# Kernel tuning notes

Hardware: AMD Instinct MI355X
Metric: run time of the kernel (lower is better)

Reference implementation:

```python
import jax, jax.numpy as jnp
import numpy as np

N = 100000      # num_nodes
E = 1600000     # num_edges (avg degree 16)
D_IN = 128
D_H = 128
D_OUT = 128


def _init_linear(key, out_dim, in_dim):
    # Kaiming-uniform-like init, bound = 1/sqrt(fan_in)
    bound = 1.0 / np.sqrt(in_dim)
    return jax.random.uniform(key, (out_dim, in_dim), jnp.float32, -bound, bound)


def setup_inputs() -> dict:
    key = jax.random.key(0)
    ks = jax.random.split(key, 12)
    x = jax.random.normal(ks[0], (N, D_IN), jnp.float32)
    edge_index = jax.random.randint(ks[1], (2, E), 0, N, jnp.int32)
    dims = [(D_H, D_IN), (D_H, D_H), (D_OUT, D_H)]
    inp = {"x": x, "edge_index": edge_index}
    for i, (do, di) in enumerate(dims):
        inp[f"Wl{i}"] = _init_linear(ks[2 + 3 * i], do, di)      # lin_l: applied to aggregated neighbors
        inp[f"bl{i}"] = jnp.zeros((do,), jnp.float32)
        inp[f"Wr{i}"] = _init_linear(ks[3 + 3 * i], do, di)      # lin_r: applied to root (self) features
    return inp


def _sage_conv(x, src, dst, Wl, bl, Wr):
    # mean aggregation of source-node features at destination nodes
    msg = x[src]                                                   # [E, d]
    agg = jax.ops.segment_sum(msg, dst, num_segments=N)            # [N, d]
    deg = jax.ops.segment_sum(jnp.ones((src.shape[0],), x.dtype), dst, num_segments=N)
    mean = agg / jnp.maximum(deg, 1.0)[:, None]
    return mean @ Wl.T + bl + x @ Wr.T


def reference(x, edge_index, Wl0, bl0, Wr0, Wl1, bl1, Wr1, Wl2, bl2, Wr2):
    src, dst = edge_index[0], edge_index[1]
    # dropout is identity in eval mode
    h = jax.nn.relu(_sage_conv(x, src, dst, Wl0, bl0, Wr0))
    h = jax.nn.relu(_sage_conv(h, src, dst, Wl1, bl1, Wr1))
    return _sage_conv(h, src, dst, Wl2, bl2, Wr2)
```

## Files before the change

### kernel.cpp

```cpp
#include <hip/hip_runtime.h>
#include <hip/hip_bf16.h>

typedef __attribute__((ext_vector_type(8))) short bf16x8;
typedef __attribute__((ext_vector_type(4))) float f32x4;

#define D 128
#define P2CAP 8192


__global__ __launch_bounds__(256) void k_setup(
    const float* __restrict__ x,
    const float* __restrict__ w0, const float* __restrict__ w1,
    const float* __restrict__ w2, const float* __restrict__ w3,
    const float* __restrict__ w4, const float* __restrict__ w5,
    __hip_bfloat16* __restrict__ xb, __hip_bfloat16* __restrict__ wb,
    int* __restrict__ bhist, int xpair)
{
    int t = blockIdx.x * 256 + threadIdx.x;
    if (t < 512) bhist[t] = 0;
    if (t < xpair) {
        float2 f = ((const float2*)x)[t];
        ((__hip_bfloat162*)xb)[t] = __float22bfloat162_rn(f);
    }
    if (t < 6 * 8192) {
        int wsel = t >> 13, wi = t & 8191;
        const float* wp = w0;
        if (wsel == 1) wp = w1;
        else if (wsel == 2) wp = w2;
        else if (wsel == 3) wp = w3;
        else if (wsel == 4) wp = w4;
        else if (wsel == 5) wp = w5;
        float2 f = ((const float2*)wp)[wi];
        ((__hip_bfloat162*)wb)[t] = __float22bfloat162_rn(f);
    }
}


__global__ __launch_bounds__(256) void k_p0(const int* __restrict__ dst,
                                            int* __restrict__ bhist, int e, int n, int epb) {
    __shared__ int lh[512];
    for (int i = threadIdx.x; i < 512; i += 256) lh[i] = 0;
    __syncthreads();
    int lo = blockIdx.x * epb;
    int hi = lo + epb; if (hi > e) hi = e;
    for (int i = lo + threadIdx.x; i < hi; i += 256) {
        int d = dst[i]; d = ((unsigned)d < (unsigned)n) ? d : 0;
        atomicAdd(&lh[d >> 8], 1);
    }
    __syncthreads();
    for (int i = threadIdx.x; i < 512; i += 256)
        if (lh[i]) atomicAdd(&bhist[i], lh[i]);
}

__global__ void k_bscan(const int* __restrict__ bhist, int* __restrict__ bbase,
                        int* __restrict__ bcursor, int nb) {
    __shared__ int lds[512];
    int t = threadIdx.x;
    int v = (t < nb) ? bhist[t] : 0;
    lds[t] = v;
    __syncthreads();
    for (int off = 1; off < 512; off <<= 1) {
        int x = (t >= off) ? lds[t - off] : 0;
        __syncthreads();
        lds[t] += x;
        __syncthreads();
    }
    if (t < nb) { int b = lds[t] - v; bbase[t] = b; bcursor[t] = b; }
    if (t == nb) bbase[t] = lds[nb - 1];
}

__global__ __launch_bounds__(256) void k_p1(const int* __restrict__ src,
                                            const int* __restrict__ dst,
                                            int* __restrict__ bcursor,
                                            int* __restrict__ tmp, int e, int n, int epb) {
    __shared__ int lh[512], gb[512];
    for (int i = threadIdx.x; i < 512; i += 256) lh[i] = 0;
    __syncthreads();
    int lo = blockIdx.x * epb;
    int hi = lo + epb; if (hi > e) hi = e;
    for (int i = lo + threadIdx.x; i < hi; i += 256) {
        int d = dst[i]; d = ((unsigned)d < (unsigned)n) ? d : 0;
        atomicAdd(&lh[d >> 8], 1);
    }
    __syncthreads();
    for (int i = threadIdx.x; i < 512; i += 256) {
        int c = lh[i];
        gb[i] = c ? atomicAdd(&bcursor[i], c) : 0;
    }
    __syncthreads();
    for (int i = threadIdx.x; i < 512; i += 256) lh[i] = 0;
    __syncthreads();
    for (int i = lo + threadIdx.x; i < hi; i += 256) {
        int d = dst[i]; d = ((unsigned)d < (unsigned)n) ? d : 0;
        int s = src[i]; s = ((unsigned)s < (unsigned)n) ? s : 0;
        int b = d >> 8;
        int p = gb[b] + atomicAdd(&lh[b], 1);
        tmp[p] = s | ((d & 255) << 17);
    }
}

__global__ __launch_bounds__(256) void k_p2(const int* __restrict__ tmp,
                                            const int* __restrict__ bbase,
                                            int* __restrict__ deg, int* __restrict__ offs,
                                            int* __restrict__ csr, int n) {
    __shared__ int hist[256], loc[256], cur[256];
    __shared__ int out[P2CAP];
    int b = blockIdx.x, t = threadIdx.x;
    int base = bbase[b];
    int cnt = bbase[b + 1] - base;
    int nodes = n - b * 256; if (nodes > 256) nodes = 256;
    hist[t] = 0;
    __syncthreads();
    for (int i = t; i < cnt; i += 256)
        atomicAdd(&hist[(tmp[base + i] >> 17) & 255], 1);
    __syncthreads();
    int v = hist[t];
    loc[t] = v;
    __syncthreads();
    for (int off = 1; off < 256; off <<= 1) {
        int x = (t >= off) ? loc[t - off] : 0;
        __syncthreads();
        loc[t] += x;
        __syncthreads();
    }
    int myloc = loc[t] - v;
    cur[t] = myloc;
    if (t < nodes) { deg[b * 256 + t] = v; offs[b * 256 + t] = base + myloc; }
    __syncthreads();
    if (cnt <= P2CAP) {
        for (int i = t; i < cnt; i += 256) {
            int e = tmp[base + i];
            int p = atomicAdd(&cur[(e >> 17) & 255], 1);
            out[p] = e & 0x1FFFF;
        }
        __syncthreads();
        for (int i = t; i < cnt; i += 256) csr[base + i] = out[i];
    } else {
        for (int i = t; i < cnt; i += 256) {
            int e = tmp[base + i];
            int p = atomicAdd(&cur[(e >> 17) & 255], 1);
            csr[base + p] = e & 0x1FFFF;
        }
    }
}


__device__ __forceinline__ void acc_int4(float* acc, int4 d) {
    acc[0] += __uint_as_float((unsigned)d.x << 16);
    acc[1] += __uint_as_float((unsigned)d.x & 0xffff0000u);
    acc[2] += __uint_as_float((unsigned)d.y << 16);
    acc[3] += __uint_as_float((unsigned)d.y & 0xffff0000u);
    acc[4] += __uint_as_float((unsigned)d.z << 16);
    acc[5] += __uint_as_float((unsigned)d.z & 0xffff0000u);
    acc[6] += __uint_as_float((unsigned)d.w << 16);
    acc[7] += __uint_as_float((unsigned)d.w & 0xffff0000u);
}

__global__ __launch_bounds__(256) void k_agg(
    const __hip_bfloat16* __restrict__ h,
    const int* __restrict__ csr,
    const int* __restrict__ offs,
    const int* __restrict__ deg,
    __hip_bfloat16* __restrict__ mean,
    int n)
{
    int node = blockIdx.x * 4 + (threadIdx.x >> 6);
    int lane = threadIdx.x & 63;
    if (node >= n) return;
    int grp = lane >> 4;
    int sub = lane & 15;
    int start = offs[node];
    int cnt = deg[node];

    float acc[8];
    #pragma unroll
    for (int k = 0; k < 8; ++k) acc[k] = 0.f;

    const char* hb = (const char*)h;
    int i = 0;
    int bulk = cnt & ~15;

    for (; i < bulk; i += 16) {
        int4 d[4];
        #pragma unroll
        for (int u = 0; u < 4; ++u) {
            int s = csr[start + i + u * 4 + grp];
            s = ((unsigned)s < (unsigned)n) ? s : 0;
            d[u] = *(const int4*)(hb + (size_t)s * 256 + sub * 16);
        }
        #pragma unroll
        for (int u = 0; u < 4; ++u) acc_int4(acc, d[u]);
    }

    if (i < cnt) {
        int4 d[4];
        #pragma unroll
        for (int u = 0; u < 4; ++u) {
            int e = i + u * 4 + grp;
            int ec = (e < cnt) ? e : (cnt - 1);
            int s = csr[start + ec];
            s = ((unsigned)s < (unsigned)n) ? s : 0;
            d[u] = *(const int4*)(hb + (size_t)s * 256 + sub * 16);
            if (e >= cnt) { d[u].x = 0; d[u].y = 0; d[u].z = 0; d[u].w = 0; }
        }
        #pragma unroll
        for (int u = 0; u < 4; ++u) acc_int4(acc, d[u]);
    }

    #pragma unroll
    for (int k = 0; k < 8; ++k) {
        acc[k] += __shfl_xor(acc[k], 16);
        acc[k] += __shfl_xor(acc[k], 32);
    }

    if (grp == 0) {
        float inv = 1.0f / fmaxf((float)cnt, 1.0f);
        union { int4 i4; __hip_bfloat162 h2[4]; } u;
        #pragma unroll
        for (int k = 0; k < 4; ++k)
            u.h2[k] = __float22bfloat162_rn(make_float2(acc[2 * k] * inv, acc[2 * k + 1] * inv));
        *(int4*)((char*)mean + (size_t)node * 256 + sub * 16) = u.i4;
    }
}


__global__ __launch_bounds__(256) void k_gemm(
    const __hip_bfloat16* __restrict__ A0,
    const __hip_bfloat16* __restrict__ A1,
    const __hip_bfloat16* __restrict__ Wb,
    const float* __restrict__ bias,
    float* __restrict__ outF,
    __hip_bfloat16* __restrict__ outB,
    int n, int do_relu)
{
    __shared__ __hip_bfloat16 lW[2 * 128 * 128];

    for (int g = threadIdx.x; g < 4096; g += 256) {
        int half = g >> 11;
        int rem  = g & 2047;
        int row  = rem >> 4;
        int c    = rem & 15;
        bf16x8 v = *(const bf16x8*)(Wb + half * 16384 + row * 128 + c * 8);
        *(bf16x8*)(lW + half * 16384 + row * 128 + ((c ^ (row & 7)) * 8)) = v;
    }
    __syncthreads();

    int w = threadIdx.x >> 6;
    int lane = threadIdx.x & 63;
    int m = lane & 15;
    int q = lane >> 4;
    int base = blockIdx.x * 256 + w * 64;

    f32x4 acc[4][8];
    #pragma unroll
    for (int r = 0; r < 4; ++r)
        #pragma unroll
        for (int i = 0; i < 8; ++i) acc[r][i] = (f32x4){0.f, 0.f, 0.f, 0.f};

    const __hip_bfloat16* Aps[2] = {A0, A1};

    #pragma unroll
    for (int half = 0; half < 2; ++half) {
        const __hip_bfloat16* A = Aps[half];
        #pragma unroll
        for (int kk = 0; kk < 4; ++kk) {
            bf16x8 af[4];
            #pragma unroll
            for (int r = 0; r < 4; ++r) {
                int arow = base + r * 16 + m;
                if (arow > n - 1) arow = n - 1;
                af[r] = *(const bf16x8*)(A + (size_t)arow * D + kk * 32 + q * 8);
            }
            #pragma unroll
            for (int nt = 0; nt < 8; ++nt) {
                int row = nt * 16 + m;
                int c = (kk * 4 + q) ^ (m & 7);
                bf16x8 bf = *(const bf16x8*)(lW + half * 16384 + row * 128 + c * 8);
                #pragma unroll
                for (int r = 0; r < 4; ++r)
                    acc[r][nt] = __builtin_amdgcn_mfma_f32_16x16x32_bf16(af[r], bf, acc[r][nt], 0, 0, 0);
            }
        }
    }

    #pragma unroll
    for (int r = 0; r < 4; ++r) {
        #pragma unroll
        for (int nt = 0; nt < 8; ++nt) {
            int col = nt * 16 + m;
            float b = bias[col];
            #pragma unroll
            for (int rr = 0; rr < 4; ++rr) {
                int row = base + r * 16 + q * 4 + rr;
                if (row < n) {
                    float v = acc[r][nt][rr] + b;
                    if (do_relu) v = fmaxf(v, 0.f);
                    if (outF) outF[(size_t)row * D + col] = v;
                    else      outB[(size_t)row * D + col] = __float2bfloat16(v);
                }
            }
        }
    }
}


extern "C" void kernel_launch(void* const* d_in, const int* in_sizes, int n_in,
                              void* d_out, int out_size, void* d_ws, size_t ws_size,
                              hipStream_t stream) {
    const float* x   = (const float*)d_in[0];
    const int*   ei  = (const int*)d_in[1];
    const float* Wl0 = (const float*)d_in[2];
    const float* bl0 = (const float*)d_in[3];
    const float* Wr0 = (const float*)d_in[4];
    const float* Wl1 = (const float*)d_in[5];
    const float* bl1 = (const float*)d_in[6];
    const float* Wr1 = (const float*)d_in[7];
    const float* Wl2 = (const float*)d_in[8];
    const float* bl2 = (const float*)d_in[9];
    const float* Wr2 = (const float*)d_in[10];

    const int n = in_sizes[0] / D;
    const int e = in_sizes[1] / 2;
    const int* src = ei;
    const int* dst = ei + e;
    const int nb = (n + 255) >> 8;

    uintptr_t p = ((uintptr_t)d_ws + 255) & ~(uintptr_t)255;
    auto carve = [&](size_t bytes) {
        uintptr_t r = p;
        p = (p + bytes + 255) & ~(uintptr_t)255;
        return (void*)r;
    };
    int* deg     = (int*)carve((size_t)n * 4);
    int* offs    = (int*)carve((size_t)n * 4);
    int* bhist   = (int*)carve(512 * 4);
    int* bbase   = (int*)carve(513 * 4);
    int* bcursor = (int*)carve(512 * 4);
    int* csr     = (int*)carve((size_t)e * 4);
    __hip_bfloat16* mean = (__hip_bfloat16*)carve((size_t)n * D * 2);
    __hip_bfloat16* F1   = (__hip_bfloat16*)carve((size_t)n * D * 2);
    __hip_bfloat16* Wb   = (__hip_bfloat16*)carve((size_t)6 * D * D * 2);
    (void)ws_size; (void)n_in; (void)out_size;

    __hip_bfloat16* h0 = (__hip_bfloat16*)d_out;
    int* tmp = (int*)((char*)d_out + (size_t)n * D * 2);

    const int xpair = n * D / 2;

    k_setup<<<(xpair + 255) / 256, 256, 0, stream>>>(
        x, Wl0, Wr0, Wl1, Wr1, Wl2, Wr2, F1, Wb, bhist, xpair);

    const int epb0 = (e + 511) / 512;
    k_p0<<<512, 256, 0, stream>>>(dst, bhist, e, n, epb0);
    k_bscan<<<1, 512, 0, stream>>>(bhist, bbase, bcursor, nb);
    const int epb1 = 8192;
    k_p1<<<(e + epb1 - 1) / epb1, 256, 0, stream>>>(src, dst, bcursor, tmp, e, n, epb1);
    k_p2<<<nb, 256, 0, stream>>>(tmp, bbase, deg, offs, csr, n);

    const int ag = (n + 3) / 4;
    const int gg = (n + 255) / 256;

    __hip_bfloat16* Wb0 = Wb + 0 * 2 * D * D;
    __hip_bfloat16* Wb1 = Wb + 1 * 2 * D * D;
    __hip_bfloat16* Wb2 = Wb + 2 * 2 * D * D;

    k_agg<<<ag, 256, 0, stream>>>(F1, csr, offs, deg, mean, n);
    k_gemm<<<gg, 256, 0, stream>>>(mean, F1, Wb0, bl0, nullptr, h0, n, 1);
    k_agg<<<ag, 256, 0, stream>>>(h0, csr, offs, deg, mean, n);
    k_gemm<<<gg, 256, 0, stream>>>(mean, h0, Wb1, bl1, nullptr, F1, n, 1);
    k_agg<<<ag, 256, 0, stream>>>(F1, csr, offs, deg, mean, n);
    k_gemm<<<gg, 256, 0, stream>>>(mean, F1, Wb2, bl2, (float*)d_out, nullptr, n, 0);
}
```

Baseline: 435.9 us.

## Fuse neighbor aggregation and dual GEMM into one kernel per layer

Merges the per-layer mean aggregation and the GEMM into a single kernel. Each 128-row tile first gathers neighbor means into padded shared memory, then runs MFMA against weights read straight from global or cache instead of staged in LDS. This removes the mean buffer's global write and re-read and three kernel launches. The cost is that each wave processes 32 nodes serially, which exposes gather latency. It also gives up the LDS-swizzled weight reuse, since every block re-reads the weights from global.

```diff
diff --git a/kernel.cpp b/kernel.cpp
--- a/kernel.cpp
+++ b/kernel.cpp
@@ -6,6 +6,8 @@
 
 #define D 128
 #define P2CAP 8192
+#define TILE 128
+#define LROW 136
 
 
 __global__ __launch_bounds__(256) void k_setup(
@@ -156,144 +158,126 @@
     acc[7] += __uint_as_float((unsigned)d.w & 0xffff0000u);
 }
 
-__global__ __launch_bounds__(256) void k_agg(
+__global__ __launch_bounds__(256, 4) void k_fused(
     const __hip_bfloat16* __restrict__ h,
     const int* __restrict__ csr,
     const int* __restrict__ offs,
     const int* __restrict__ deg,
-    __hip_bfloat16* __restrict__ mean,
-    int n)
-{
-    int node = blockIdx.x * 4 + (threadIdx.x >> 6);
-    int lane = threadIdx.x & 63;
-    if (node >= n) return;
-    int grp = lane >> 4;
-    int sub = lane & 15;
-    int start = offs[node];
-    int cnt = deg[node];
-
-    float acc[8];
-    #pragma unroll
-    for (int k = 0; k < 8; ++k) acc[k] = 0.f;
-
-    const char* hb = (const char*)h;
-    int i = 0;
-    int bulk = cnt & ~15;
-
-    for (; i < bulk; i += 16) {
-        int4 d[4];
-        #pragma unroll
-        for (int u = 0; u < 4; ++u) {
-            int s = csr[start + i + u * 4 + grp];
-            s = ((unsigned)s < (unsigned)n) ? s : 0;
-            d[u] = *(const int4*)(hb + (size_t)s * 256 + sub * 16);
-        }
-        #pragma unroll
-        for (int u = 0; u < 4; ++u) acc_int4(acc, d[u]);
-    }
-
-    if (i < cnt) {
-        int4 d[4];
-        #pragma unroll
-        for (int u = 0; u < 4; ++u) {
-            int e = i + u * 4 + grp;
-            int ec = (e < cnt) ? e : (cnt - 1);
-            int s = csr[start + ec];
-            s = ((unsigned)s < (unsigned)n) ? s : 0;
-            d[u] = *(const int4*)(hb + (size_t)s * 256 + sub * 16);
-            if (e >= cnt) { d[u].x = 0; d[u].y = 0; d[u].z = 0; d[u].w = 0; }
-        }
-        #pragma unroll
-        for (int u = 0; u < 4; ++u) acc_int4(acc, d[u]);
-    }
-
-    #pragma unroll
-    for (int k = 0; k < 8; ++k) {
-        acc[k] += __shfl_xor(acc[k], 16);
-        acc[k] += __shfl_xor(acc[k], 32);
-    }
-
-    if (grp == 0) {
-        float inv = 1.0f / fmaxf((float)cnt, 1.0f);
-        union { int4 i4; __hip_bfloat162 h2[4]; } u;
-        #pragma unroll
-        for (int k = 0; k < 4; ++k)
-            u.h2[k] = __float22bfloat162_rn(make_float2(acc[2 * k] * inv, acc[2 * k + 1] * inv));
-        *(int4*)((char*)mean + (size_t)node * 256 + sub * 16) = u.i4;
-    }
-}
-
-
-__global__ __launch_bounds__(256) void k_gemm(
-    const __hip_bfloat16* __restrict__ A0,
-    const __hip_bfloat16* __restrict__ A1,
     const __hip_bfloat16* __restrict__ Wb,
     const float* __restrict__ bias,
     float* __restrict__ outF,
     __hip_bfloat16* __restrict__ outB,
     int n, int do_relu)
 {
-    __shared__ __hip_bfloat16 lW[2 * 128 * 128];
-
-    for (int g = threadIdx.x; g < 4096; g += 256) {
-        int half = g >> 11;
-        int rem  = g & 2047;
-        int row  = rem >> 4;
-        int c    = rem & 15;
-        bf16x8 v = *(const bf16x8*)(Wb + half * 16384 + row * 128 + c * 8);
-        *(bf16x8*)(lW + half * 16384 + row * 128 + ((c ^ (row & 7)) * 8)) = v;
-    }
-    __syncthreads();
+    __shared__ __hip_bfloat16 lM[TILE * LROW];
 
     int w = threadIdx.x >> 6;
     int lane = threadIdx.x & 63;
+    int grp = lane >> 4;
+    int sub = lane & 15;
+    int base = blockIdx.x * TILE;
+    const char* hb = (const char*)h;
+
+    for (int it = 0; it < 32; ++it) {
+        int rl = w * 32 + it;
+        int node = base + rl;
+        float acc[8];
+        #pragma unroll
+        for (int k = 0; k < 8; ++k) acc[k] = 0.f;
+        int cnt = 0, start = 0;
+        if (node < n) { start = offs[node]; cnt = deg[node]; }
+
+        int i = 0, bulk = cnt & ~15;
+        for (; i < bulk; i += 16) {
+            int4 d[4];
+            #pragma unroll
+            for (int u = 0; u < 4; ++u) {
+                int s = csr[start + i + u * 4 + grp];
+                s = ((unsigned)s < (unsigned)n) ? s : 0;
+                d[u] = *(const int4*)(hb + (size_t)s * 256 + sub * 16);
+            }
+            #pragma unroll
+            for (int u = 0; u < 4; ++u) acc_int4(acc, d[u]);
+        }
+        if (i < cnt) {
+            int4 d[4];
+            #pragma unroll
+            for (int u = 0; u < 4; ++u) {
+                int e = i + u * 4 + grp;
+                int ec = (e < cnt) ? e : (cnt - 1);
+                int s = csr[start + ec];
+                s = ((unsigned)s < (unsigned)n) ? s : 0;
+                d[u] = *(const int4*)(hb + (size_t)s * 256 + sub * 16);
+                if (e >= cnt) { d[u].x = 0; d[u].y = 0; d[u].z = 0; d[u].w = 0; }
+            }
+            #pragma unroll
+            for (int u = 0; u < 4; ++u) acc_int4(acc, d[u]);
+        }
+
+        #pragma unroll
+        for (int k = 0; k < 8; ++k) {
+            acc[k] += __shfl_xor(acc[k], 16);
+            acc[k] += __shfl_xor(acc[k], 32);
+        }
+
+        if (grp == 0) {
+            float inv = 1.0f / fmaxf((float)cnt, 1.0f);
+            union { int4 i4; __hip_bfloat162 h2[4]; } u;
+            #pragma unroll
+            for (int k = 0; k < 4; ++k)
+                u.h2[k] = __float22bfloat162_rn(make_float2(acc[2 * k] * inv, acc[2 * k + 1] * inv));
+            *(int4*)((char*)lM + (size_t)rl * (LROW * 2) + sub * 16) = u.i4;
+        }
+    }
+    __syncthreads();
+
     int m = lane & 15;
     int q = lane >> 4;
-    int base = blockIdx.x * 256 + w * 64;
-
-    f32x4 acc[4][8];
+    int rbase = w * 32;
+
+    f32x4 acc2[2][8];
     #pragma unroll
-    for (int r = 0; r < 4; ++r)
-        #pragma unroll
-        for (int i = 0; i < 8; ++i) acc[r][i] = (f32x4){0.f, 0.f, 0.f, 0.f};
-
-    const __hip_bfloat16* Aps[2] = {A0, A1};
+    for (int r = 0; r < 2; ++r)
+        #pragma unroll
+        for (int i = 0; i < 8; ++i) acc2[r][i] = (f32x4){0.f, 0.f, 0.f, 0.f};
 
     #pragma unroll
     for (int half = 0; half < 2; ++half) {
-        const __hip_bfloat16* A = Aps[half];
         #pragma unroll
         for (int kk = 0; kk < 4; ++kk) {
-            bf16x8 af[4];
-            #pragma unroll
-            for (int r = 0; r < 4; ++r) {
-                int arow = base + r * 16 + m;
-                if (arow > n - 1) arow = n - 1;
-                af[r] = *(const bf16x8*)(A + (size_t)arow * D + kk * 32 + q * 8);
+            bf16x8 af[2];
+            #pragma unroll
+            for (int r = 0; r < 2; ++r) {
+                int rl = rbase + r * 16 + m;
+                if (half == 0) {
+                    af[r] = *(const bf16x8*)((const char*)lM + (size_t)rl * (LROW * 2) + (kk * 4 + q) * 16);
+                } else {
+                    int arow = base + rl;
+                    if (arow > n - 1) arow = n - 1;
+                    af[r] = *(const bf16x8*)(h + (size_t)arow * D + kk * 32 + q * 8);
+                }
             }
             #pragma unroll
             for (int nt = 0; nt < 8; ++nt) {
-                int row = nt * 16 + m;
-                int c = (kk * 4 + q) ^ (m & 7);
-                bf16x8 bf = *(const bf16x8*)(lW + half * 16384 + row * 128 + c * 8);
+                bf16x8 bf = *(const bf16x8*)(Wb + half * 16384 + (size_t)(nt * 16 + m) * D + kk * 32 + q * 8);
                 #pragma unroll
-                for (int r = 0; r < 4; ++r)
-                    acc[r][nt] = __builtin_amdgcn_mfma_f32_16x16x32_bf16(af[r], bf, acc[r][nt], 0, 0, 0);
+                for (int r = 0; r < 2; ++r)
+                    acc2[r][nt] = __builtin_amdgcn_mfma_f32_16x16x32_bf16(af[r], bf, acc2[r][nt], 0, 0, 0);
             }
         }
     }
 
     #pragma unroll
-    for (int r = 0; r < 4; ++r) {
+    for (int r = 0; r < 2; ++r) {
         #pragma unroll
         for (int nt = 0; nt < 8; ++nt) {
             int col = nt * 16 + m;
             float b = bias[col];
             #pragma unroll
             for (int rr = 0; rr < 4; ++rr) {
-                int row = base + r * 16 + q * 4 + rr;
+                int row = base + rbase + r * 16 + q * 4 + rr;
                 if (row < n) {
-                    float v = acc[r][nt][rr] + b;
+                    float v = acc2[r][nt][rr] + b;
                     if (do_relu) v = fmaxf(v, 0.f);
                     if (outF) outF[(size_t)row * D + col] = v;
                     else      outB[(size_t)row * D + col] = __float2bfloat16(v);
@@ -337,9 +321,8 @@
     int* bbase   = (int*)carve(513 * 4);
     int* bcursor = (int*)carve(512 * 4);
     int* csr     = (int*)carve((size_t)e * 4);
-    __hip_bfloat16* mean = (__hip_bfloat16*)carve((size_t)n * D * 2);
-    __hip_bfloat16* F1   = (__hip_bfloat16*)carve((size_t)n * D * 2);
-    __hip_bfloat16* Wb   = (__hip_bfloat16*)carve((size_t)6 * D * D * 2);
+    __hip_bfloat16* F1 = (__hip_bfloat16*)carve((size_t)n * D * 2);
+    __hip_bfloat16* Wb = (__hip_bfloat16*)carve((size_t)6 * D * D * 2);
     (void)ws_size; (void)n_in; (void)out_size;
 
     __hip_bfloat16* h0 = (__hip_bfloat16*)d_out;
@@ -357,17 +340,13 @@
     k_p1<<<(e + epb1 - 1) / epb1, 256, 0, stream>>>(src, dst, bcursor, tmp, e, n, epb1);
     k_p2<<<nb, 256, 0, stream>>>(tmp, bbase, deg, offs, csr, n);
 
-    const int ag = (n + 3) / 4;
-    const int gg = (n + 255) / 256;
+    const int fg = (n + TILE - 1) / TILE;
 
     __hip_bfloat16* Wb0 = Wb + 0 * 2 * D * D;
     __hip_bfloat16* Wb1 = Wb + 1 * 2 * D * D;
     __hip_bfloat16* Wb2 = Wb + 2 * 2 * D * D;
 
-    k_agg<<<ag, 256, 0, stream>>>(F1, csr, offs, deg, mean, n);
-    k_gemm<<<gg, 256, 0, stream>>>(mean, F1, Wb0, bl0, nullptr, h0, n, 1);
-    k_agg<<<ag, 256, 0, stream>>>(h0, csr, offs, deg, mean, n);
-    k_gemm<<<gg, 256, 0, stream>>>(mean, h0, Wb1, bl1, nullptr, F1, n, 1);
-    k_agg<<<ag, 256, 0, stream>>>(F1, csr, offs, deg, mean, n);
-    k_gemm<<<gg, 256, 0, stream>>>(mean, F1, Wb2, bl2, (float*)d_out, nullptr, n, 0);
-}
+    k_fused<<<fg, 256, 0, stream>>>(F1, csr, offs, deg, Wb0, bl0, nullptr, h0, n, 1);
+    k_fused<<<fg, 256, 0, stream>>>(h0, csr, offs, deg, Wb1, bl1, nullptr, F1, n, 1);
+    k_fused<<<fg, 256, 0, stream>>>(F1, csr, offs, deg, Wb2, bl2, (float*)d_out, nullptr, n, 0);
+}
```

Result: slower. 492.5 us (+13.0%).
